# Kernel tuning notes

Hardware: AMD Instinct MI355X
Metric: run time of the kernel (lower is better)

Reference implementation:

```python
import jax, jax.numpy as jnp
import numpy as np

RES = 128
SH_DIM = 9            # (deg+1)^2, deg=2
CH = SH_DIM * 3 + 1   # 28: 3*9 SH rgb coeffs + 1 sigma
AABB_MIN = -1.0
AABB_MAX = 1.0
STEP = (AABB_MAX - AABB_MIN) / (RES - 1)   # voxel_len = mean(aabb_size/(res-1))
UNIFORM = 0.5
N_SAMPLES = int(RES * 3 / UNIFORM)         # plenoxels count: 768
EPS = 1e-10


def sh_encode_deg2(d):
    # real spherical harmonics basis, degree 2 (9 coefficients), on normalized dirs
    d = d / jnp.linalg.norm(d, axis=-1, keepdims=True)
    x, y, z = d[..., 0], d[..., 1], d[..., 2]
    C0 = 0.28209479177387814
    C1 = 0.4886025119029199
    C20, C21, C22 = 1.0925484305920792, -1.0925484305920792, 0.31539156525252005
    C23, C24 = -1.0925484305920792, 0.5462742152960396
    return jnp.stack([
        jnp.full_like(x, C0),
        -C1 * y, C1 * z, -C1 * x,
        C20 * x * y, C21 * y * z, C22 * (2.0 * z * z - x * x - y * y),
        C23 * x * z, C24 * (x * x - y * y),
    ], axis=-1)


def grid_sample_3d(grid, pts):
    # grid: [D,H,W,C]; pts: [...,3] in [-1,1], (x,y,z) with x->W, y->H, z->D.
    # Matches torch F.grid_sample(mode='bilinear', padding_mode='zeros', align_corners=True).
    D, H, W, C = grid.shape
    lead = pts.shape[:-1]
    p = pts.reshape(-1, 3)
    x = (p[:, 0] + 1.0) * 0.5 * (W - 1)
    y = (p[:, 1] + 1.0) * 0.5 * (H - 1)
    z = (p[:, 2] + 1.0) * 0.5 * (D - 1)
    x0f, y0f, z0f = jnp.floor(x), jnp.floor(y), jnp.floor(z)
    fx, fy, fz = x - x0f, y - y0f, z - z0f
    x0 = x0f.astype(jnp.int32)
    y0 = y0f.astype(jnp.int32)
    z0 = z0f.astype(jnp.int32)
    flat = grid.reshape(-1, C)
    out = jnp.zeros((p.shape[0], C), grid.dtype)
    for dz in (0, 1):
        for dy in (0, 1):
            for dx in (0, 1):
                xi, yi, zi = x0 + dx, y0 + dy, z0 + dz
                valid = (xi >= 0) & (xi < W) & (yi >= 0) & (yi < H) & (zi >= 0) & (zi < D)
                w = ((fx if dx else 1.0 - fx)
                     * (fy if dy else 1.0 - fy)
                     * (fz if dz else 1.0 - fz)) * valid
                idx = (jnp.clip(zi, 0, D - 1) * H + jnp.clip(yi, 0, H - 1)) * W + jnp.clip(xi, 0, W - 1)
                out = out + w[:, None] * flat[idx]
    return out.reshape(lead + (C,))


def setup_inputs() -> dict:
    key = jax.random.key(0)
    k1, k2, k3 = jax.random.split(key, 3)
    B = 4096
    # origins on a radius-3 sphere, aimed at jittered targets inside the unit box
    o = jax.random.normal(k1, (B, 3), dtype=jnp.float32)
    rays_o = 3.0 * o / jnp.linalg.norm(o, axis=-1, keepdims=True)
    tgt = jax.random.uniform(k2, (B, 3), dtype=jnp.float32, minval=-0.5, maxval=0.5)
    d = tgt - rays_o
    rays_d = d / jnp.linalg.norm(d, axis=-1, keepdims=True)
    grid_data = 0.1 * jax.random.normal(k3, (RES ** 3, CH), dtype=jnp.float32)
    grid_data = grid_data.at[:, -1].add(0.1)  # ini_sigma offset
    return {"rays_d": rays_d, "rays_o": rays_o, "grid_data": grid_data}


def reference(rays_d, rays_o, grid_data):
    B = rays_d.shape[0]
    aabb_lo = jnp.full((3,), AABB_MIN, rays_o.dtype)
    aabb_hi = jnp.full((3,), AABB_MAX, rays_o.dtype)
    # ray-AABB intersection (no_grad in torch)
    t_pos = (aabb_hi - rays_o) / rays_d
    t_neg = (aabb_lo - rays_o) / rays_d
    t_in = jnp.minimum(t_pos, t_neg)
    t_out = jnp.maximum(t_pos, t_neg)
    start = jnp.max(t_in, axis=-1)                  # [B]
    stop = jnp.min(t_out, axis=-1, keepdims=True)   # [B,1]
    # tensor_linspace from start+u*step to start+u*step*n, then clamp max=stop
    w = jnp.linspace(0.0, 1.0, N_SAMPLES, dtype=rays_o.dtype)  # [S]
    s0 = start + UNIFORM * STEP
    s1 = start + UNIFORM * STEP * N_SAMPLES
    intersections = s0[:, None] * (1.0 - w) + s1[:, None] * w   # [B,S]
    intersections = jnp.minimum(intersections, stop)
    t = intersections[:, :-1]                                    # [B,S-1]
    pts = rays_o[:, None, :] + t[:, :, None] * rays_d[:, None, :]
    pts = (pts - AABB_MIN) * (2.0 / (AABB_MAX - AABB_MIN)) - 1.0  # normalize to [-1,1]
    # trilinear sample of the voxel grid (torch layout: D=res0,H=res1,W=res2; x->W)
    interp = grid_sample_3d(grid_data.reshape(RES, RES, RES, CH), pts)  # [B,S-1,CH]
    sigma = interp[..., -1]
    rgb_sh = interp[..., :-1].reshape(B, N_SAMPLES - 1, 3, SH_DIM)
    sh = sh_encode_deg2(rays_d)                                   # [B,9]
    rgb = jnp.einsum('bsck,bk->bsc', rgb_sh, sh)
    # volumetric rendering
    dists = jnp.diff(intersections, axis=1) * jnp.linalg.norm(rays_d, axis=-1, keepdims=True)
    alpha = 1.0 - jnp.exp(-jax.nn.relu(sigma) * dists)
    cum_light = jnp.concatenate(
        [jnp.ones((B, 1), alpha.dtype), jnp.cumprod(1.0 - alpha[:, :-1] + EPS, axis=-1)], axis=-1)
    abs_light = alpha * cum_light
    acc_map = abs_light.sum(-1)
    rgb_map = (abs_light[..., None] * jax.nn.sigmoid(rgb)).sum(-2)
    depth = (abs_light * t).sum(-1)
    rgb_map = rgb_map + (1.0 - acc_map[:, None])  # white background
    return rgb_map, alpha, depth
```

## Files before the change

### kernel.cpp

```cpp
#include <hip/hip_runtime.h>
#include <math.h>

#define RESG 128
#define CHG 28
#define NT 767
#define NLBKT 48

template <int PAT>
static __device__ __forceinline__ float swz(float x) {
    return __int_as_float(__builtin_amdgcn_ds_swizzle(__float_as_int(x), PAT));
}

__global__ __launch_bounds__(1024) void prep_sort(
    const float* __restrict__ rays_d, const float* __restrict__ rays_o,
    int* __restrict__ perm, int B)
{
    __shared__ int cnt[64];
    __shared__ int off[64];
    __shared__ unsigned char keys[4096];
    const int tid = threadIdx.x;
    if (tid < 64) cnt[tid] = 0;
    __syncthreads();
    for (int r = tid; r < B; r += 1024) {
        const float ox = rays_o[r*3+0], oy = rays_o[r*3+1], oz = rays_o[r*3+2];
        const float dx = rays_d[r*3+0], dy = rays_d[r*3+1], dz = rays_d[r*3+2];
        float txp = (1.0f - ox)/dx, txn = (-1.0f - ox)/dx;
        float typ = (1.0f - oy)/dy, tyn = (-1.0f - oy)/dy;
        float tzp = (1.0f - oz)/dz, tzn = (-1.0f - oz)/dz;
        const float start = fmaxf(fmaxf(fminf(txp,txn), fminf(typ,tyn)), fminf(tzp,tzn));
        const float stop  = fminf(fminf(fmaxf(txp,txn), fmaxf(typ,tyn)), fmaxf(tzp,tzn));
        int n_proc = (int)((stop - start) * 127.0f) + 2;
        n_proc = n_proc < 0 ? 0 : (n_proc > NT ? NT : n_proc);
        int lvl = n_proc >> 4; if (lvl > NLBKT-1) lvl = NLBKT-1;
        const int k = (NLBKT-1) - lvl;
        keys[r] = (unsigned char)k;
        atomicAdd(&cnt[k], 1);
    }
    __syncthreads();
    if (tid < 64) {
        int v = cnt[tid];
        int incl = v;
        #pragma unroll
        for (int o2 = 1; o2 < 64; o2 <<= 1) {
            const int n = __shfl_up(incl, o2, 64);
            if ((tid & 63) >= o2) incl += n;
        }
        off[tid] = incl - v;
    }
    __syncthreads();
    for (int r = tid; r < B; r += 1024) {
        const int slot = atomicAdd(&off[keys[r]], 1);
        perm[slot] = r;
    }
}

__global__ __launch_bounds__(256) void nerf_grid_kernel(
    const float* __restrict__ rays_d,
    const float* __restrict__ rays_o,
    const float* __restrict__ grid,
    const int*   __restrict__ perm,
    float* __restrict__ out_rgb,
    float* __restrict__ out_alpha,
    float* __restrict__ out_depth)
{
    const int ray  = perm[blockIdx.x];
    const int tid  = threadIdx.x;
    const int lane = tid & 63;
    const int wave = tid >> 6;

    const float EPSC   = 1e-10f;
    const float INV127 = 1.0f / 127.0f;

    __shared__ float a_lds[NT + 1];
    __shared__ float r_lds[NT + 1];
    __shared__ float g_lds[NT + 1];
    __shared__ float b_lds[NT + 1];
    __shared__ float sh_lds[12];
    __shared__ float wprod[4];
    __shared__ float red[4][5];

    const float ox = rays_o[ray*3+0], oy = rays_o[ray*3+1], oz = rays_o[ray*3+2];
    const float dx = rays_d[ray*3+0], dy = rays_d[ray*3+1], dz = rays_d[ray*3+2];
    const float dnorm = sqrtf(dx*dx + dy*dy + dz*dz);

    float txp = (1.0f - ox)/dx, txn = (-1.0f - ox)/dx;
    float typ = (1.0f - oy)/dy, tyn = (-1.0f - oy)/dy;
    float tzp = (1.0f - oz)/dz, tzn = (-1.0f - oz)/dz;
    const float start = fmaxf(fmaxf(fminf(txp,txn), fminf(typ,tyn)), fminf(tzp,tzn));
    const float stop  = fminf(fminf(fmaxf(txp,txn), fmaxf(typ,tyn)), fmaxf(tzp,tzn));

    int n_proc = (int)((stop - start) * 127.0f) + 2;
    n_proc = n_proc < 0 ? 0 : (n_proc > NT ? NT : n_proc);

    const float inv = 1.0f/dnorm;
    const float nx = dx*inv, ny = dy*inv, nz = dz*inv;
    {
        const float C0 = 0.28209479177387814f;
        const float C1 = 0.4886025119029199f;
        const float C20 = 1.0925484305920792f, C21 = -1.0925484305920792f;
        const float C22 = 0.31539156525252005f;
        const float C23 = -1.0925484305920792f, C24 = 0.5462742152960396f;
        if (tid == 0) {
            sh_lds[0] = C0;
            sh_lds[1] = -C1*ny;
            sh_lds[2] =  C1*nz;
            sh_lds[3] = -C1*nx;
            sh_lds[4] = C20*nx*ny;
            sh_lds[5] = C21*ny*nz;
            sh_lds[6] = C22*(2.0f*nz*nz - nx*nx - ny*ny);
            sh_lds[7] = C23*nx*nz;
            sh_lds[8] = C24*(nx*nx - ny*ny);
            sh_lds[9] = 0.0f; sh_lds[10] = 0.0f; sh_lds[11] = 0.0f;
        }
    }
    __syncthreads();

    const int samp = lane >> 3;
    const int j    = lane & 7;
    float cR[4], cG[4], cB[4];
    #pragma unroll
    for (int m = 0; m < 4; ++m) {
        const int ch = 4*j + m;
        const int iR = ch      > 11 ? 11 : ch;
        const int iG = (ch-9)  < 0 ? 0 : ((ch-9)  > 11 ? 11 : (ch-9));
        const int iB = (ch-18) < 0 ? 0 : ((ch-18) > 11 ? 11 : (ch-18));
        cR[m] = (ch < 9)               ? sh_lds[iR] : 0.0f;
        cG[m] = (ch >= 9 && ch < 18)   ? sh_lds[iG] : 0.0f;
        cB[m] = (ch >= 18 && ch < 27)  ? sh_lds[iB] : 0.0f;
    }
    const float cS3 = (j == 6) ? 1.0f : 0.0f;
    const int chunk_off = (j < 7 ? j : 6) << 4;
    const char* gridc = (const char*)grid;

    for (int base = wave*8; base < n_proc; base += 32) {
        const int s = base + samp;
        const float t0 = fminf(start + (float)(s+1)*INV127, stop);
        const float t1 = fminf(start + (float)(s+2)*INV127, stop);
        const float dist = (t1 - t0) * dnorm;
        const bool live = (s < n_proc) && (dist > 0.0f);

        const float gx = fminf(fmaxf((ox + t0*dx + 1.0f)*63.5f, 0.0f), 127.0f);
        const float gy = fminf(fmaxf((oy + t0*dy + 1.0f)*63.5f, 0.0f), 127.0f);
        const float gz = fminf(fmaxf((oz + t0*dz + 1.0f)*63.5f, 0.0f), 127.0f);
        const float fx0 = floorf(gx), fy0 = floorf(gy), fz0 = floorf(gz);
        const float fx = gx - fx0, fy = gy - fy0, fz = gz - fz0;
        const int ix = (int)fx0, iy = (int)fy0, iz = (int)fz0;

        const int Bv = ((iz*RESG + iy)*RESG + ix)*112 + chunk_off;
        const int offx = (ix < RESG-1) ? 112 : 0;
        const int offy = (iy < RESG-1) ? 112*RESG : 0;
        const int offz = (iz < RESG-1) ? 112*RESG*RESG : 0;
        int offs[8];
        offs[0] = 0;           offs[1] = offx;
        offs[2] = offy;        offs[3] = offx + offy;
        offs[4] = offz;        offs[5] = offz + offx;
        offs[6] = offz + offy; offs[7] = offz + offx + offy;

        const float liveF = live ? 1.0f : 0.0f;
        const float wx1 = fx, wx0 = 1.0f - fx;
        const float wy1 = fy, wy0 = 1.0f - fy;
        const float wz1 = fz*liveF, wz0 = (1.0f - fz)*liveF;
        const float w00 = wx0*wy0, w10 = wx1*wy0, w01 = wx0*wy1, w11 = wx1*wy1;
        float wc[8];
        wc[0] = w00*wz0; wc[1] = w10*wz0; wc[2] = w01*wz0; wc[3] = w11*wz0;
        wc[4] = w00*wz1; wc[5] = w10*wz1; wc[6] = w01*wz1; wc[7] = w11*wz1;

        float av0 = 0.0f, av1 = 0.0f, av2 = 0.0f, av3 = 0.0f;
        #pragma unroll
        for (int i = 0; i < 8; ++i) {
            const float4 v = *(const float4*)(gridc + (size_t)(unsigned)(Bv + offs[i]));
            av0 = fmaf(wc[i], v.x, av0);
            av1 = fmaf(wc[i], v.y, av1);
            av2 = fmaf(wc[i], v.z, av2);
            av3 = fmaf(wc[i], v.w, av3);
        }

        float rr = av0*cR[0] + av1*cR[1] + av2*cR[2] + av3*cR[3];
        float gg = av0*cG[0] + av1*cG[1] + av2*cG[2] + av3*cG[3];
        float bb = av0*cB[0] + av1*cB[1] + av2*cB[2] + av3*cB[3];
        float sg = av3*cS3;

        rr += swz<0x041F>(rr); gg += swz<0x041F>(gg); bb += swz<0x041F>(bb); sg += swz<0x041F>(sg);
        rr += swz<0x081F>(rr); gg += swz<0x081F>(gg); bb += swz<0x081F>(bb); sg += swz<0x081F>(sg);
        rr += swz<0x101F>(rr); gg += swz<0x101F>(gg); bb += swz<0x101F>(bb); sg += swz<0x101F>(sg);

        if (j == 0 && s < n_proc) {
            a_lds[s] = 1.0f - expf(-fmaxf(sg, 0.0f)*dist);
            r_lds[s] = 1.0f/(1.0f + expf(-rr));
            g_lds[s] = 1.0f/(1.0f + expf(-gg));
            b_lds[s] = 1.0f/(1.0f + expf(-bb));
        }
    }
    __syncthreads();

    for (int s = tid; s < NT; s += 256)
        out_alpha[(size_t)ray*NT + s] = (s < n_proc) ? a_lds[s] : 0.0f;

    float a_r[3], q_r[3], t_r[3], rr_r[3], gg_r[3], bb_r[3];
    #pragma unroll
    for (int k = 0; k < 3; ++k) {
        const int s = tid*3 + k;
        float a = 0.0f, rr = 0.0f, gg = 0.0f, bb = 0.0f, tt = 0.0f;
        if (s < NT) {
            tt = fminf(start + (float)(s+1)*INV127, stop);
            if (s < n_proc) {
                a = a_lds[s];
                rr = r_lds[s]; gg = g_lds[s]; bb = b_lds[s];
            }
        }
        a_r[k] = a; q_r[k] = (s < NT) ? (1.0f - a + EPSC) : 1.0f;
        t_r[k] = tt; rr_r[k] = rr; gg_r[k] = gg; bb_r[k] = bb;
    }

    const float P = q_r[0]*q_r[1]*q_r[2];
    float incl = P;
    #pragma unroll
    for (int off2 = 1; off2 < 64; off2 <<= 1) {
        const float n = __shfl_up(incl, off2, 64);
        if (lane >= off2) incl *= n;
    }
    float excl = __shfl_up(incl, 1, 64);
    if (lane == 0) excl = 1.0f;

    if (lane == 63) wprod[wave] = incl;
    __syncthreads();
    float wpre = 1.0f;
    for (int w2 = 0; w2 < 4; ++w2) if (w2 < wave) wpre *= wprod[w2];

    float cum = wpre * excl;
    float accA = 0.0f, accR = 0.0f, accG = 0.0f, accB = 0.0f, accD = 0.0f;
    #pragma unroll
    for (int k = 0; k < 3; ++k) {
        const float abs_l = a_r[k] * cum;
        accA += abs_l;
        accR += abs_l * rr_r[k];
        accG += abs_l * gg_r[k];
        accB += abs_l * bb_r[k];
        accD += abs_l * t_r[k];
        cum *= q_r[k];
    }

    #pragma unroll
    for (int off2 = 32; off2 > 0; off2 >>= 1) {
        accA += __shfl_down(accA, off2, 64);
        accR += __shfl_down(accR, off2, 64);
        accG += __shfl_down(accG, off2, 64);
        accB += __shfl_down(accB, off2, 64);
        accD += __shfl_down(accD, off2, 64);
    }
    if (lane == 0) {
        red[wave][0] = accA; red[wave][1] = accR; red[wave][2] = accG;
        red[wave][3] = accB; red[wave][4] = accD;
    }
    __syncthreads();
    if (tid == 0) {
        float A = 0.0f, R = 0.0f, G = 0.0f, Bv2 = 0.0f, D = 0.0f;
        #pragma unroll
        for (int w2 = 0; w2 < 4; ++w2) {
            A += red[w2][0]; R += red[w2][1]; G += red[w2][2];
            Bv2 += red[w2][3]; D += red[w2][4];
        }
        const float bg = 1.0f - A;
        out_rgb[ray*3+0] = R   + bg;
        out_rgb[ray*3+1] = G   + bg;
        out_rgb[ray*3+2] = Bv2 + bg;
        out_depth[ray] = D;
    }
}

extern "C" void kernel_launch(void* const* d_in, const int* in_sizes, int n_in,
                              void* d_out, int out_size, void* d_ws, size_t ws_size,
                              hipStream_t stream) {
    const float* rays_d = (const float*)d_in[0];
    const float* rays_o = (const float*)d_in[1];
    const float* grid   = (const float*)d_in[2];
    const int B = in_sizes[0] / 3;

    float* out       = (float*)d_out;
    float* out_rgb   = out;
    float* out_alpha = out + (size_t)B*3;
    float* out_depth = out + (size_t)B*3 + (size_t)B*NT;

    int* perm = (int*)d_ws;

    prep_sort<<<1, 1024, 0, stream>>>(rays_d, rays_o, perm, B);
    nerf_grid_kernel<<<B, 256, 0, stream>>>(rays_d, rays_o, grid, perm,
                                            out_rgb, out_alpha, out_depth);
}
```

Baseline: 87.56 us.

## Use one wave per ray with streaming transmittance scan instead of LDS staging

Each ray is now processed by a single 64-lane wave instead of a 256-thread block. Alpha and color are composited on the fly, using an in-wave product scan over the 8 samples per iteration and a running transmittance carried across iterations. This removes the LDS arrays, the block barriers and the separate post-pass scan. The trade-off is less parallelism per ray and a serial chain across iterations. The grid gathers per wave now run sequentially over all samples, which could lengthen per-ray latency unless higher occupancy hides it.

```diff
diff --git a/kernel.cpp b/kernel.cpp
--- a/kernel.cpp
+++ b/kernel.cpp
@@ -54,7 +54,7 @@
     }
 }
 
-__global__ __launch_bounds__(256) void nerf_grid_kernel(
+__global__ __launch_bounds__(64) void nerf_grid_kernel(
     const float* __restrict__ rays_d,
     const float* __restrict__ rays_o,
     const float* __restrict__ grid,
@@ -64,20 +64,10 @@
     float* __restrict__ out_depth)
 {
     const int ray  = perm[blockIdx.x];
-    const int tid  = threadIdx.x;
-    const int lane = tid & 63;
-    const int wave = tid >> 6;
+    const int lane = threadIdx.x & 63;
 
     const float EPSC   = 1e-10f;
     const float INV127 = 1.0f / 127.0f;
-
-    __shared__ float a_lds[NT + 1];
-    __shared__ float r_lds[NT + 1];
-    __shared__ float g_lds[NT + 1];
-    __shared__ float b_lds[NT + 1];
-    __shared__ float sh_lds[12];
-    __shared__ float wprod[4];
-    __shared__ float red[4][5];
 
     const float ox = rays_o[ray*3+0], oy = rays_o[ray*3+1], oz = rays_o[ray*3+2];
     const float dx = rays_d[ray*3+0], dy = rays_d[ray*3+1], dz = rays_d[ray*3+2];
@@ -94,26 +84,18 @@
 
     const float inv = 1.0f/dnorm;
     const float nx = dx*inv, ny = dy*inv, nz = dz*inv;
+    float sh[9];
     {
         const float C0 = 0.28209479177387814f;
         const float C1 = 0.4886025119029199f;
         const float C20 = 1.0925484305920792f, C21 = -1.0925484305920792f;
         const float C22 = 0.31539156525252005f;
         const float C23 = -1.0925484305920792f, C24 = 0.5462742152960396f;
-        if (tid == 0) {
-            sh_lds[0] = C0;
-            sh_lds[1] = -C1*ny;
-            sh_lds[2] =  C1*nz;
-            sh_lds[3] = -C1*nx;
-            sh_lds[4] = C20*nx*ny;
-            sh_lds[5] = C21*ny*nz;
-            sh_lds[6] = C22*(2.0f*nz*nz - nx*nx - ny*ny);
-            sh_lds[7] = C23*nx*nz;
-            sh_lds[8] = C24*(nx*nx - ny*ny);
-            sh_lds[9] = 0.0f; sh_lds[10] = 0.0f; sh_lds[11] = 0.0f;
-        }
-    }
-    __syncthreads();
+        sh[0] = C0;   sh[1] = -C1*ny; sh[2] = C1*nz; sh[3] = -C1*nx;
+        sh[4] = C20*nx*ny; sh[5] = C21*ny*nz;
+        sh[6] = C22*(2.0f*nz*nz - nx*nx - ny*ny);
+        sh[7] = C23*nx*nz; sh[8] = C24*(nx*nx - ny*ny);
+    }
 
     const int samp = lane >> 3;
     const int j    = lane & 7;
@@ -121,18 +103,20 @@
     #pragma unroll
     for (int m = 0; m < 4; ++m) {
         const int ch = 4*j + m;
-        const int iR = ch      > 11 ? 11 : ch;
-        const int iG = (ch-9)  < 0 ? 0 : ((ch-9)  > 11 ? 11 : (ch-9));
-        const int iB = (ch-18) < 0 ? 0 : ((ch-18) > 11 ? 11 : (ch-18));
-        cR[m] = (ch < 9)               ? sh_lds[iR] : 0.0f;
-        cG[m] = (ch >= 9 && ch < 18)   ? sh_lds[iG] : 0.0f;
-        cB[m] = (ch >= 18 && ch < 27)  ? sh_lds[iB] : 0.0f;
+        cR[m] = (ch < 9)              ? sh[ch]    : 0.0f;
+        cG[m] = (ch >= 9 && ch < 18)  ? sh[ch-9]  : 0.0f;
+        cB[m] = (ch >= 18 && ch < 27) ? sh[ch-18] : 0.0f;
     }
     const float cS3 = (j == 6) ? 1.0f : 0.0f;
     const int chunk_off = (j < 7 ? j : 6) << 4;
     const char* gridc = (const char*)grid;
 
-    for (int base = wave*8; base < n_proc; base += 32) {
+    const size_t rayNT = (size_t)ray * NT;
+
+    float T = 1.0f;
+    float accA = 0.0f, accR = 0.0f, accG = 0.0f, accB = 0.0f, accD = 0.0f;
+
+    for (int base = 0; base < n_proc; base += 8) {
         const int s = base + samp;
         const float t0 = fminf(start + (float)(s+1)*INV127, stop);
         const float t1 = fminf(start + (float)(s+2)*INV127, stop);
@@ -184,87 +168,58 @@
         rr += swz<0x081F>(rr); gg += swz<0x081F>(gg); bb += swz<0x081F>(bb); sg += swz<0x081F>(sg);
         rr += swz<0x101F>(rr); gg += swz<0x101F>(gg); bb += swz<0x101F>(bb); sg += swz<0x101F>(sg);
 
-        if (j == 0 && s < n_proc) {
-            a_lds[s] = 1.0f - expf(-fmaxf(sg, 0.0f)*dist);
-            r_lds[s] = 1.0f/(1.0f + expf(-rr));
-            g_lds[s] = 1.0f/(1.0f + expf(-gg));
-            b_lds[s] = 1.0f/(1.0f + expf(-bb));
-        }
-    }
-    __syncthreads();
-
-    for (int s = tid; s < NT; s += 256)
-        out_alpha[(size_t)ray*NT + s] = (s < n_proc) ? a_lds[s] : 0.0f;
-
-    float a_r[3], q_r[3], t_r[3], rr_r[3], gg_r[3], bb_r[3];
-    #pragma unroll
-    for (int k = 0; k < 3; ++k) {
-        const int s = tid*3 + k;
-        float a = 0.0f, rr = 0.0f, gg = 0.0f, bb = 0.0f, tt = 0.0f;
-        if (s < NT) {
-            tt = fminf(start + (float)(s+1)*INV127, stop);
-            if (s < n_proc) {
-                a = a_lds[s];
-                rr = r_lds[s]; gg = g_lds[s]; bb = b_lds[s];
-            }
-        }
-        a_r[k] = a; q_r[k] = (s < NT) ? (1.0f - a + EPSC) : 1.0f;
-        t_r[k] = tt; rr_r[k] = rr; gg_r[k] = gg; bb_r[k] = bb;
-    }
-
-    const float P = q_r[0]*q_r[1]*q_r[2];
-    float incl = P;
-    #pragma unroll
-    for (int off2 = 1; off2 < 64; off2 <<= 1) {
-        const float n = __shfl_up(incl, off2, 64);
-        if (lane >= off2) incl *= n;
-    }
-    float excl = __shfl_up(incl, 1, 64);
-    if (lane == 0) excl = 1.0f;
-
-    if (lane == 63) wprod[wave] = incl;
-    __syncthreads();
-    float wpre = 1.0f;
-    for (int w2 = 0; w2 < 4; ++w2) if (w2 < wave) wpre *= wprod[w2];
-
-    float cum = wpre * excl;
-    float accA = 0.0f, accR = 0.0f, accG = 0.0f, accB = 0.0f, accD = 0.0f;
-    #pragma unroll
-    for (int k = 0; k < 3; ++k) {
-        const float abs_l = a_r[k] * cum;
+        const float a = live ? (1.0f - expf(-fmaxf(sg, 0.0f)*dist)) : 0.0f;
+        const float q = (s < n_proc) ? (1.0f - a + EPSC) : 1.0f;
+        const float r1 = 1.0f/(1.0f + expf(-rr));
+        const float g1 = 1.0f/(1.0f + expf(-gg));
+        const float b1 = 1.0f/(1.0f + expf(-bb));
+
+        float incl = q;
+        { const float n = __shfl_up(incl,  8, 64); if (lane >=  8) incl *= n; }
+        { const float n = __shfl_up(incl, 16, 64); if (lane >= 16) incl *= n; }
+        { const float n = __shfl_up(incl, 32, 64); if (lane >= 32) incl *= n; }
+        float excl = __shfl_up(incl, 8, 64);
+        if (lane < 8) excl = 1.0f;
+
+        const float abs_l = a * T * excl;
         accA += abs_l;
-        accR += abs_l * rr_r[k];
-        accG += abs_l * gg_r[k];
-        accB += abs_l * bb_r[k];
-        accD += abs_l * t_r[k];
-        cum *= q_r[k];
-    }
-
-    #pragma unroll
-    for (int off2 = 32; off2 > 0; off2 >>= 1) {
-        accA += __shfl_down(accA, off2, 64);
-        accR += __shfl_down(accR, off2, 64);
-        accG += __shfl_down(accG, off2, 64);
-        accB += __shfl_down(accB, off2, 64);
-        accD += __shfl_down(accD, off2, 64);
-    }
+        accR += abs_l * r1;
+        accG += abs_l * g1;
+        accB += abs_l * b1;
+        accD += abs_l * t0;
+
+        const float a_out = __shfl(a, (lane & 7) * 8, 64);
+        if (lane < 8 && base + lane < n_proc)
+            out_alpha[rayNT + base + lane] = a_out;
+
+        T *= __shfl(incl, 56, 64);
+    }
+
+    for (int s2 = n_proc + lane; s2 < NT; s2 += 64)
+        out_alpha[rayNT + s2] = 0.0f;
+
+    accA += __shfl_down(accA,  8, 64);
+    accR += __shfl_down(accR,  8, 64);
+    accG += __shfl_down(accG,  8, 64);
+    accB += __shfl_down(accB,  8, 64);
+    accD += __shfl_down(accD,  8, 64);
+    accA += __shfl_down(accA, 16, 64);
+    accR += __shfl_down(accR, 16, 64);
+    accG += __shfl_down(accG, 16, 64);
+    accB += __shfl_down(accB, 16, 64);
+    accD += __shfl_down(accD, 16, 64);
+    accA += __shfl_down(accA, 32, 64);
+    accR += __shfl_down(accR, 32, 64);
+    accG += __shfl_down(accG, 32, 64);
+    accB += __shfl_down(accB, 32, 64);
+    accD += __shfl_down(accD, 32, 64);
+
     if (lane == 0) {
-        red[wave][0] = accA; red[wave][1] = accR; red[wave][2] = accG;
-        red[wave][3] = accB; red[wave][4] = accD;
-    }
-    __syncthreads();
-    if (tid == 0) {
-        float A = 0.0f, R = 0.0f, G = 0.0f, Bv2 = 0.0f, D = 0.0f;
-        #pragma unroll
-        for (int w2 = 0; w2 < 4; ++w2) {
-            A += red[w2][0]; R += red[w2][1]; G += red[w2][2];
-            Bv2 += red[w2][3]; D += red[w2][4];
-        }
-        const float bg = 1.0f - A;
-        out_rgb[ray*3+0] = R   + bg;
-        out_rgb[ray*3+1] = G   + bg;
-        out_rgb[ray*3+2] = Bv2 + bg;
-        out_depth[ray] = D;
+        const float bg = 1.0f - accA;
+        out_rgb[ray*3+0] = accR + bg;
+        out_rgb[ray*3+1] = accG + bg;
+        out_rgb[ray*3+2] = accB + bg;
+        out_depth[ray] = accD;
     }
 }
 
@@ -284,6 +239,6 @@
     int* perm = (int*)d_ws;
 
     prep_sort<<<1, 1024, 0, stream>>>(rays_d, rays_o, perm, B);
-    nerf_grid_kernel<<<B, 256, 0, stream>>>(rays_d, rays_o, grid, perm,
-                                            out_rgb, out_alpha, out_depth);
-}
+    nerf_grid_kernel<<<B, 64, 0, stream>>>(rays_d, rays_o, grid, perm,
+                                           out_rgb, out_alpha, out_depth);
+}
```

After: 96.95 us. +10.7%, slower.
